# Kernel tuning notes

Hardware: AMD Instinct MI355X
Metric: run time of the kernel (lower is better)

## Reference

```python
import jax, jax.numpy as jnp
import numpy as np

N, E = 3200, 50000
RBF, HID = 16, 128
CUT = 5.0
NS, NV = 32, 16            # multiplicities of 0e and 1o blocks
D = NS + 3 * NV            # 80 = node/message irrep dim
WNUM = NS*NS + NV*NS + NS*NV + NV*NV  # 2304 tensor-product weights per edge
EPS = 1e-8
# path normalization (fully-connected TP, 2 paths per output irrep)
A1 = 1.0 / np.sqrt(2.0 * NS)
A2 = 1.0 / np.sqrt(2.0 * NV)
A3 = 1.0 / np.sqrt(2.0 * NS)
A4 = 1.0 / np.sqrt(2.0 * NV)
ISQ3 = 1.0 / np.sqrt(3.0)


def setup_inputs() -> dict:
    key = jax.random.key(0)
    ks = jax.random.split(key, 24)
    nrm = lambda k, s, sc=1.0: jax.random.normal(k, s, jnp.float32) * sc
    x = nrm(ks[0], (N, D))
    edge_src = jax.random.randint(ks[1], (E,), 0, N)
    edge_dst = jax.random.randint(ks[2], (E,), 0, N)
    dirs = nrm(ks[3], (E, 3))
    unit = dirs / jnp.linalg.norm(dirs, axis=1, keepdims=True)
    # component-normalized SH for l=0,1: [1, sqrt(3)*r_hat]
    edge_sh = jnp.concatenate([jnp.ones((E, 1), jnp.float32), np.sqrt(3.0) * unit], axis=1)
    edge_rbf = nrm(ks[4], (E, RBF))
    edge_len = jax.random.uniform(ks[5], (E,), jnp.float32, 0.1, 6.0)  # some beyond cutoff
    inp = dict(x=x, edge_src=edge_src, edge_dst=edge_dst, edge_sh=edge_sh,
               edge_rbf=edge_rbf, edge_len=edge_len)
    # IrrepNorm affine params
    inp['norm_w'] = jnp.ones((D,), jnp.float32)
    inp['norm_b'] = jnp.zeros((D,), jnp.float32)
    # radial weight MLP (RBF -> HID -> HID -> WNUM)
    inp['mw1'] = nrm(ks[6], (RBF, HID), 1.0/np.sqrt(RBF)); inp['mb1'] = jnp.zeros((HID,), jnp.float32)
    inp['mw2'] = nrm(ks[7], (HID, HID), 1.0/np.sqrt(HID)); inp['mb2'] = jnp.zeros((HID,), jnp.float32)
    inp['mw3'] = nrm(ks[8], (HID, WNUM), 1.0/np.sqrt(HID)); inp['mb3'] = jnp.zeros((WNUM,), jnp.float32)
    # edge gate MLP (RBF -> HID -> 1)
    inp['gw1'] = nrm(ks[9], (RBF, HID), 1.0/np.sqrt(RBF)); inp['gb1'] = jnp.zeros((HID,), jnp.float32)
    inp['gw2'] = nrm(ks[10], (HID, 1), 1.0/np.sqrt(HID)); inp['gb2'] = jnp.zeros((1,), jnp.float32)
    # equivariant linears (e3nn stores N(0,1) weights, normalizes by 1/sqrt(fan_in))
    inp['Ws'] = nrm(ks[11], (NS, NS + NV))   # msg_linear scalar part: 32 -> 32 scalars + 16 gates
    inp['Wv'] = nrm(ks[12], (NV, NV))        # msg_linear vector part
    inp['Us'] = nrm(ks[13], (NS, NS))        # update_linear
    inp['Uv'] = nrm(ks[14], (NV, NV))
    inp['Ss'] = nrm(ks[15], (NS, NS))        # self_linear
    inp['Sv'] = nrm(ks[16], (NV, NV))
    inp['res_scale'] = jnp.float32(0.1)
    return inp


def _irrep_norm(x, w, b):
    s = x[:, :NS]
    v = x[:, NS:].reshape(-1, NV, 3)
    mean = s.mean(axis=1, keepdims=True)
    var = ((s - mean) ** 2).mean(axis=1, keepdims=True)
    s = (s - mean) / jnp.sqrt(var + EPS)
    rms = jnp.sqrt((v ** 2).mean(axis=2, keepdims=True) + EPS)
    v = v / rms
    out = jnp.concatenate([s, v.reshape(-1, 3 * NV)], axis=-1)
    return out * w + b


def reference(x, edge_src, edge_dst, edge_sh, edge_rbf, edge_len,
              norm_w, norm_b, mw1, mb1, mw2, mb2, mw3, mb3,
              gw1, gb1, gw2, gb2, Ws, Wv, Us, Uv, Ss, Sv, res_scale):
    silu = jax.nn.silu
    x_norm = _irrep_norm(x, norm_w, norm_b)                  # [N, 80]
    # radial tensor-product weights per edge
    h = silu(edge_rbf @ mw1 + mb1)
    h = silu(h @ mw2 + mb2)
    tpw = h @ mw3 + mb3                                      # [E, 2304]
    o1 = NS*NS; o2 = o1 + NV*NS; o3 = o2 + NS*NV
    w1 = tpw[:, :o1].reshape(-1, NS, NS)
    w2 = tpw[:, o1:o2].reshape(-1, NV, NS)
    w3 = tpw[:, o2:o3].reshape(-1, NS, NV)
    w4 = tpw[:, o3:].reshape(-1, NV, NV)
    # gather source node features
    xs = x_norm[edge_src, :NS]                               # [E, 32]
    xv = x_norm[edge_src, NS:].reshape(-1, NV, 3)            # [E, 16, 3]
    sh0 = edge_sh[:, 0]                                      # [E]
    sh1 = edge_sh[:, 1:4]                                    # [E, 3]
    # fully-connected TP paths
    msg_s = A1 * jnp.einsum('ei,eio->eo', xs * sh0[:, None], w1)
    inner = jnp.einsum('eim,em->ei', xv, sh1) * ISQ3         # 1o x 1o -> 0e
    msg_s = msg_s + A2 * jnp.einsum('ei,eio->eo', inner, w2)
    msg_v = A3 * jnp.einsum('ei,eio->eo', xs, w3)[:, :, None] * sh1[:, None, :]
    msg_v = msg_v + A4 * jnp.einsum('eim,eio->eom', xv, w4) * sh0[:, None, None]
    m = jnp.concatenate([msg_s, msg_v.reshape(-1, 3 * NV)], axis=-1)  # [E, 80]
    # cutoff envelope and learned edge gate
    cutoff_w = 0.5 * (jnp.cos(jnp.pi * edge_len / CUT) + 1.0) * (edge_len <= CUT).astype(x.dtype)
    gate_w = jax.nn.sigmoid(silu(edge_rbf @ gw1 + gb1) @ gw2 + gb2)   # [E, 1]
    edge_w = cutoff_w[:, None] * gate_w                               # [E, 1]
    m = m * edge_w
    # scatter-add aggregate + normalization
    agg = jax.ops.segment_sum(m, edge_dst, num_segments=N)            # [N, 80]
    den = jax.ops.segment_sum(edge_w, edge_dst, num_segments=N)       # [N, 1]
    agg = agg / jnp.maximum(den, 1e-8)
    # msg_linear -> scalars + gates + gated vectors
    ag_s = agg[:, :NS]
    ag_v = agg[:, NS:].reshape(-1, NV, 3)
    sc = (ag_s @ Ws) / np.sqrt(NS)                                    # [N, 48]
    vc = jnp.einsum('nim,io->nom', ag_v, Wv) / np.sqrt(NV)            # [N, 16, 3]
    s_g = silu(sc[:, :NS])
    gates = jax.nn.sigmoid(sc[:, NS:])
    v_g = vc * gates[:, :, None]
    # update + self interaction
    upd_s = (s_g @ Us) / np.sqrt(NS)
    upd_v = jnp.einsum('nim,io->nom', v_g, Uv) / np.sqrt(NV)
    self_s = (x_norm[:, :NS] @ Ss) / np.sqrt(NS)
    self_v = jnp.einsum('nim,io->nom', x_norm[:, NS:].reshape(-1, NV, 3), Sv) / np.sqrt(NV)
    out = jnp.concatenate([self_s + upd_s, (self_v + upd_v).reshape(-1, 3 * NV)], axis=-1)
    return x + res_scale * out
```

## Files before the change

### kernel.cpp

```cpp
#include <hip/hip_runtime.h>
#include <hip/hip_bf16.h>
#include <math.h>

#define N_NODES 3200
#define E_EDGES 50000
#define RBFN 16
#define HID 128
#define NS 32
#define NV 16
#define DD 80
#define WNUM 2304
#define CUTF 5.0f
#define EPSF 1e-8f

#define A1C 0.125f
#define A2C 0.17677669529663687f
#define A3C 0.125f
#define A4C 0.17677669529663687f
#define A2ISQ 0.10206207261596575f

typedef __attribute__((ext_vector_type(4))) float f32x4;
typedef __attribute__((ext_vector_type(8))) short bf16x8;

__device__ __forceinline__ float sigm(float x) { return 1.0f / (1.0f + __expf(-x)); }
__device__ __forceinline__ float silu_f(float x) { return x * sigm(x); }

__device__ __forceinline__ short bf16r(float x) {
    union { float f; unsigned u; } v; v.f = x;
    unsigned r = (v.u + 0x7fffu + ((v.u >> 16) & 1u)) >> 16;
    return (short)r;
}
__device__ __forceinline__ float b2f(unsigned short s) {
    union { float f; unsigned u; } v; v.u = ((unsigned)s) << 16; return v.f;
}

__global__ void k_scan(const int* __restrict__ hist, int* __restrict__ start) {
    __shared__ int part[256];
    int t = threadIdx.x;
    int loc[13];
    int s = 0;
#pragma unroll
    for (int j = 0; j < 13; j++) {
        int idx = t * 13 + j;
        int v = (idx < N_NODES) ? hist[idx] : 0;
        loc[j] = s; s += v;
    }
    part[t] = s;
    __syncthreads();
    for (int off = 1; off < 256; off <<= 1) {
        int v = part[t];
        int add = (t >= off) ? part[t - off] : 0;
        __syncthreads();
        part[t] = v + add;
        __syncthreads();
    }
    int pre = (t == 0) ? 0 : part[t - 1];
#pragma unroll
    for (int j = 0; j < 13; j++) {
        int idx = t * 13 + j;
        if (idx < N_NODES) start[idx] = pre + loc[j];
    }
    if (t == 255) start[N_NODES] = part[255];
}

__global__ void k_scatter(const int* __restrict__ edst, const int* __restrict__ start,
                          int* __restrict__ cur, int* __restrict__ perm) {
    int e = blockIdx.x * 256 + threadIdx.x;
    if (e < E_EDGES) {
        int d = edst[e];
        int pos = start[d] + atomicAdd(&cur[d], 1);
        perm[pos] = e;
    }
}

__global__ void k_prep0(const float* __restrict__ mw2, __hip_bfloat16* __restrict__ mw2f) {
    __shared__ __hip_bfloat16 st[2048];
    int t = blockIdx.x, tid = threadIdx.x;
    for (int idx = tid; idx < 2048; idx += 256) {
        int k = idx >> 4, c = idx & 15;
        float v = mw2[k * HID + t * 16 + c];
        int kk = k >> 5, q4 = (k >> 3) & 3, j = k & 7;
        st[kk * 512 + (q4 * 16 + c) * 8 + j] = __float2bfloat16(v);
    }
    __syncthreads();
    ((bf16x8*)(mw2f + t * 2048))[tid] = ((const bf16x8*)st)[tid];
}

__global__ __launch_bounds__(256) void k_front(
    const float* __restrict__ rbf, const float* __restrict__ elen,
    const int* __restrict__ edst,
    const float* __restrict__ mw1, const float* __restrict__ mb1,
    const float* __restrict__ gw1, const float* __restrict__ gb1,
    const float* __restrict__ gw2, const float* __restrict__ gb2,
    const float* __restrict__ mb2, const __hip_bfloat16* __restrict__ mw2f,
    const float* __restrict__ mw3, const float* __restrict__ mb3,
    const float* __restrict__ x, const float* __restrict__ nw, const float* __restrict__ nb,
    float* __restrict__ ewg, __hip_bfloat16* __restrict__ h2b,
    __hip_bfloat16* __restrict__ mw3f, __hip_bfloat16* __restrict__ biasf,
    float* __restrict__ xn, int* __restrict__ hist) {
    __shared__ __align__(16) char smem[16640];
    int b = blockIdx.x, tid = threadIdx.x;
    if (b < 782) {
        __hip_bfloat16* h1l = (__hip_bfloat16*)smem;
        int wid = __builtin_amdgcn_readfirstlane(tid >> 6);
        int lane = tid & 63;
        int base = b * 64;
        int eb = base + wid * 16;
        {
            int c0 = lane, c1 = 64 + lane;
            float t0[16], t1[16], g0[16], g1[16];
            float b0 = mb1[c0], b1 = mb1[c1], gb0v = gb1[c0], gb1v = gb1[c1];
#pragma unroll
            for (int e = 0; e < 16; e++) { t0[e] = b0; t1[e] = b1; g0[e] = gb0v; g1[e] = gb1v; }
#pragma unroll
            for (int r = 0; r < RBFN; r++) {
                float w0 = mw1[r * HID + c0], w1 = mw1[r * HID + c1];
                float v0 = gw1[r * HID + c0], v1 = gw1[r * HID + c1];
#pragma unroll
                for (int e = 0; e < 16; e++) {
                    int ee = eb + e; if (ee >= E_EDGES) ee = E_EDGES - 1;
                    float rv = rbf[ee * RBFN + r];
                    t0[e] += rv * w0; t1[e] += rv * w1;
                    g0[e] += rv * v0; g1[e] += rv * v1;
                }
            }
            float q0 = gw2[c0], q1 = gw2[c1];
            float gb2v = gb2[0];
#pragma unroll
            for (int e = 0; e < 16; e++) {
                int le = wid * 16 + e;
                h1l[le * 128 + c0] = __float2bfloat16(silu_f(t0[e]));
                h1l[le * 128 + c1] = __float2bfloat16(silu_f(t1[e]));
                float p = silu_f(g0[e]) * q0 + silu_f(g1[e]) * q1;
                p += __shfl_xor(p, 1);  p += __shfl_xor(p, 2);  p += __shfl_xor(p, 4);
                p += __shfl_xor(p, 8);  p += __shfl_xor(p, 16); p += __shfl_xor(p, 32);
                if (lane == 0 && eb + e < E_EDGES) {
                    float len = elen[eb + e];
                    float cut = (len <= CUTF) ? 0.5f * (cosf(3.14159265358979f * len / CUTF) + 1.0f) : 0.f;
                    ewg[eb + e] = cut * sigm(p + gb2v);
                }
            }
        }
        __syncthreads();
        {
            int q4 = lane >> 4, l15 = lane & 15;
            int le = wid * 16 + l15;
            bf16x8 af[4];
#pragma unroll
            for (int kk = 0; kk < 4; kk++)
                af[kk] = *(const bf16x8*)(h1l + le * 128 + kk * 32 + q4 * 8);
            const f32x4 zf = {0.f, 0.f, 0.f, 0.f};
#pragma unroll
            for (int ct = 0; ct < 8; ct++) {
                f32x4 acc = zf;
#pragma unroll
                for (int kk = 0; kk < 4; kk++) {
                    bf16x8 bw = *(const bf16x8*)(mw2f + (ct * 4 + kk) * 512 + lane * 8);
                    acc = __builtin_amdgcn_mfma_f32_16x16x32_bf16(af[kk], bw, acc, 0, 0, 0);
                }
                float bias = mb2[ct * 16 + l15];
#pragma unroll
                for (int r = 0; r < 4; r++) {
                    int ge = base + wid * 16 + q4 * 4 + r;
                    if (ge < E_EDGES)
                        h2b[ge * HID + ct * 16 + l15] = __float2bfloat16(silu_f(acc[r] + bias));
                }
            }
        }
    } else if (b < 927) {
        int b2 = b - 782;
        __hip_bfloat16* st = (__hip_bfloat16*)smem;
        if (b2 < 144) {
            for (int idx = tid; idx < 2048; idx += 256) {
                int k = idx >> 4, c = idx & 15;
                float v = mw3[k * WNUM + b2 * 16 + c];
                int kk = k >> 5, q4 = (k >> 3) & 3, j = k & 7;
                st[kk * 512 + (q4 * 16 + c) * 8 + j] = __float2bfloat16(v);
            }
            __syncthreads();
            ((bf16x8*)(mw3f + b2 * 2048))[tid] = ((const bf16x8*)st)[tid];
        } else {
            for (int idx = tid; idx < 3072; idx += 256) {
                float val;
                if (idx < 1024) {
                    int oh = idx >> 9, l = (idx >> 3) & 63, j = idx & 7;
                    int o = oh * 16 + (l & 15), i = (l >> 4) * 8 + j;
                    val = mb3[i * 32 + o];
                } else if (idx < 2048) {
                    int t = idx - 1024;
                    int oh = t >> 9, l = (t >> 3) & 63, j = t & 7;
                    int o = oh * 16 + (l & 15), i = (l >> 4) * 8 + j;
                    val = (i < 16) ? mb3[1024 + i * 32 + o] : 0.f;
                } else if (idx < 2560) {
                    int t = idx - 2048;
                    int l = t >> 3, j = t & 7;
                    int o = l & 15, i = (l >> 4) * 8 + j;
                    val = mb3[1536 + i * 16 + o];
                } else {
                    int t = idx - 2560;
                    int l = t >> 3, j = t & 7;
                    int o = l & 15, i = (l >> 4) * 8 + j;
                    val = (i < 16) ? mb3[2048 + i * 16 + o] : 0.f;
                }
                biasf[idx] = __float2bfloat16(val);
            }
        }
    } else if (b < 1727) {
        float* row = (float*)smem;
        int sub = tid >> 6, t = tid & 63;
        int n = (b - 927) * 4 + sub;
        float* rw = row + sub * 80;
        const float* xr = x + n * DD;
        rw[t] = xr[t];
        if (t < 16) rw[64 + t] = xr[64 + t];
        __syncthreads();
        float mean = 0.f;
#pragma unroll
        for (int i = 0; i < NS; i++) mean += rw[i];
        mean *= (1.0f / NS);
        float var = 0.f;
#pragma unroll
        for (int i = 0; i < NS; i++) { float d = rw[i] - mean; var += d * d; }
        var *= (1.0f / NS);
        float inv = rsqrtf(var + EPSF);
        if (t < NS) xn[n * DD + t] = (rw[t] - mean) * inv * nw[t] + nb[t];
        if (t < 48) {
            int j = t / 3;
            float v0 = rw[NS + 3 * j], v1 = rw[NS + 3 * j + 1], v2 = rw[NS + 3 * j + 2];
            float rms = sqrtf((v0 * v0 + v1 * v1 + v2 * v2) * (1.0f / 3.0f) + EPSF);
            xn[n * DD + NS + t] = rw[NS + t] / rms * nw[NS + t] + nb[NS + t];
        }
    } else {
        int e = (b - 1727) * 256 + tid;
        if (e < E_EDGES) atomicAdd(&hist[edst[e]], 1);
    }
}

__global__ __launch_bounds__(256) void k_msg(
    const float* __restrict__ xn, const __hip_bfloat16* __restrict__ h2b,
    const float* __restrict__ ewg, const int* __restrict__ esrc,
    const int* __restrict__ edst, const int* __restrict__ perm,
    const float* __restrict__ esh,
    const __hip_bfloat16* __restrict__ mw3f, const __hip_bfloat16* __restrict__ biasf,
    const int* __restrict__ startp, float* __restrict__ agg, float* __restrict__ den) {
    __shared__ __align__(16) char pool[46080];
    unsigned short (*xng)[82]  = (unsigned short(*)[82])(pool);
    unsigned short (*innr)[16] = (unsigned short(*)[16])(pool + 20992);
    f32x4* lb0  = (f32x4*)(pool + 25088);
    f32x4* lb1  = (f32x4*)(pool + 25088 + 8192);
    float (*sh1l)[4] = (float(*)[4])(pool + 41472);
    float* sh0l = (float*)(pool + 43520);
    float* ewl  = (float*)(pool + 44032);
    int* dstl   = (int*)(pool + 44544);
    int* srcl   = (int*)(pool + 45056);
    int* gel    = (int*)(pool + 45568);
    float* msgl = (float*)(pool);

    const int tid = threadIdx.x;
    const int wid = __builtin_amdgcn_readfirstlane(tid >> 6);
    const int lane = tid & 63;
    const int q4 = lane >> 4;
    const int l15 = lane & 15;
    const int ib = q4 * 8;
    const int role = blockIdx.x & 1;
    const int e0 = (blockIdx.x >> 1) * 128;

    if (tid < 128) {
        int slot = e0 + tid;
        bool v = slot < E_EDGES;
        int ge = v ? perm[slot] : 0;
        gel[tid] = ge;
        srcl[tid] = esrc[ge];
        dstl[tid] = v ? edst[ge] : -1;
        ewl[tid] = v ? ewg[ge] : 0.f;
        sh0l[tid] = esh[ge * 4];
        sh1l[tid][0] = esh[ge * 4 + 1];
        sh1l[tid][1] = esh[ge * 4 + 2];
        sh1l[tid][2] = esh[ge * 4 + 3];
    }
    __syncthreads();
    for (int idx = tid; idx < 128 * 80; idx += 256) {
        int e = idx / 80, q = idx - e * 80;
        xng[e][q] = (unsigned short)bf16r(xn[srcl[e] * 80 + q]);
    }
    __syncthreads();
    if (role == 0) {
        for (int idx = tid; idx < 128 * 16; idx += 256) {
            int e = idx >> 4, i = idx & 15;
            float d = b2f(xng[e][32 + 3 * i]) * sh1l[e][0]
                    + b2f(xng[e][32 + 3 * i + 1]) * sh1l[e][1]
                    + b2f(xng[e][32 + 3 * i + 2]) * sh1l[e][2];
            innr[e][i] = (unsigned short)bf16r(A2ISQ * d);
        }
    }
    __syncthreads();

    int el[2] = { wid * 32 + l15, wid * 32 + 16 + l15 };
    bf16x8 hfr[2][4];
#pragma unroll
    for (int et = 0; et < 2; et++) {
        int ge = gel[el[et]];
        const __hip_bfloat16* hr = h2b + ge * HID;
#pragma unroll
        for (int kk = 0; kk < 4; kk++)
            hfr[et][kk] = *(const bf16x8*)(hr + kk * 32 + ib);
    }
    const f32x4 zf = {0.f, 0.f, 0.f, 0.f};
    float f1[2], f4e[2];
    f32x4 msgS[2][2], q3[2], qv[3][2];
    if (role == 0) {
#pragma unroll
        for (int et = 0; et < 2; et++) {
            f1[et] = A1C * sh0l[el[et]];
            bf16x8 p18, p28;
#pragma unroll
            for (int j = 0; j < 8; j++) {
                p18[j] = bf16r(b2f(xng[el[et]][ib + j]) * f1[et]);
                p28[j] = (ib + j < 16) ? (short)innr[el[et]][ib + j] : (short)0;
            }
            bf16x8 ba1a = *(const bf16x8*)(biasf + lane * 8);
            bf16x8 ba1b = *(const bf16x8*)(biasf + 512 + lane * 8);
            bf16x8 ba2a = *(const bf16x8*)(biasf + 1024 + lane * 8);
            bf16x8 ba2b = *(const bf16x8*)(biasf + 1536 + lane * 8);
            f32x4 a0 = __builtin_amdgcn_mfma_f32_16x16x32_bf16(ba1a, p18, zf, 0, 0, 0);
            msgS[0][et] = __builtin_amdgcn_mfma_f32_16x16x32_bf16(ba2a, p28, a0, 0, 0, 0);
            f32x4 a1 = __builtin_amdgcn_mfma_f32_16x16x32_bf16(ba1b, p18, zf, 0, 0, 0);
            msgS[1][et] = __builtin_amdgcn_mfma_f32_16x16x32_bf16(ba2b, p28, a1, 0, 0, 0);
        }
    } else {
#pragma unroll
        for (int et = 0; et < 2; et++) {
            f4e[et] = A4C * sh0l[el[et]];
            bf16x8 xs8;
#pragma unroll
            for (int j = 0; j < 8; j++) xs8[j] = (short)xng[el[et]][ib + j];
            bf16x8 ba3 = *(const bf16x8*)(biasf + 2048 + lane * 8);
            bf16x8 ba4 = *(const bf16x8*)(biasf + 2560 + lane * 8);
            q3[et] = __builtin_amdgcn_mfma_f32_16x16x32_bf16(ba3, xs8, zf, 0, 0, 0);
#pragma unroll
            for (int m = 0; m < 3; m++) {
                bf16x8 t8;
#pragma unroll
                for (int j = 0; j < 8; j++) {
                    int i = ib + j;
                    t8[j] = (i < 16) ? (short)xng[el[et]][32 + 3 * i + m] : (short)0;
                }
                qv[m][et] = __builtin_amdgcn_mfma_f32_16x16x32_bf16(ba4, t8, zf, 0, 0, 0);
            }
        }
    }

    const f32x4* gsrc = (const f32x4*)mw3f;

    auto compute_chunk = [&](int n, const __hip_bfloat16* bb) {
        f32x4 acc[2][2];
#pragma unroll
        for (int half = 0; half < 2; half++) {
            f32x4 a0 = zf, a1 = zf;
#pragma unroll
            for (int kk = 0; kk < 4; kk++) {
                bf16x8 af = *(const bf16x8*)(bb + ((half * 4 + kk) * 64 + lane) * 8);
                a0 = __builtin_amdgcn_mfma_f32_16x16x32_bf16(af, hfr[0][kk], a0, 0, 0, 0);
                a1 = __builtin_amdgcn_mfma_f32_16x16x32_bf16(af, hfr[1][kk], a1, 0, 0, 0);
            }
            acc[half][0] = a0; acc[half][1] = a1;
        }
        if (n < 32) {
            float p0 = f1[0] * b2f(xng[el[0]][n]);
            float p1 = f1[1] * b2f(xng[el[1]][n]);
#pragma unroll
            for (int half = 0; half < 2; half++)
#pragma unroll
                for (int r = 0; r < 4; r++) {
                    msgS[half][0][r] += p0 * acc[half][0][r];
                    msgS[half][1][r] += p1 * acc[half][1][r];
                }
        } else if (n < 48) {
            float p0 = b2f(innr[el[0]][n - 32]);
            float p1 = b2f(innr[el[1]][n - 32]);
#pragma unroll
            for (int half = 0; half < 2; half++)
#pragma unroll
                for (int r = 0; r < 4; r++) {
                    msgS[half][0][r] += p0 * acc[half][0][r];
                    msgS[half][1][r] += p1 * acc[half][1][r];
                }
        } else if (n < 64) {
#pragma unroll
            for (int half = 0; half < 2; half++) {
                int i = 2 * (n - 48) + half;
                float p0 = b2f(xng[el[0]][i]);
                float p1 = b2f(xng[el[1]][i]);
#pragma unroll
                for (int r = 0; r < 4; r++) {
                    q3[0][r] += p0 * acc[half][0][r];
                    q3[1][r] += p1 * acc[half][1][r];
                }
            }
        } else {
#pragma unroll
            for (int half = 0; half < 2; half++) {
                int i = 2 * (n - 64) + half;
#pragma unroll
                for (int m = 0; m < 3; m++) {
                    float p0 = b2f(xng[el[0]][32 + 3 * i + m]);
                    float p1 = b2f(xng[el[1]][32 + 3 * i + m]);
#pragma unroll
                    for (int r = 0; r < 4; r++) {
                        qv[m][0][r] += p0 * acc[half][0][r];
                        qv[m][1][r] += p1 * acc[half][1][r];
                    }
                }
            }
        }
    };

    const int n0 = role ? 48 : 0;
    const int n1 = role ? 72 : 48;
    f32x4 rg0, rg1;
    rg0 = gsrc[n0 * 512 + tid];
    rg1 = gsrc[n0 * 512 + 256 + tid];
    {
        f32x4* wb = (n0 & 1) ? lb1 : lb0;
        wb[tid] = rg0; wb[tid + 256] = rg1;
        if (n0 + 1 < n1) {
            rg0 = gsrc[(n0 + 1) * 512 + tid];
            rg1 = gsrc[(n0 + 1) * 512 + 256 + tid];
        }
    }
    for (int n = n0; n < n1; n++) {
        __syncthreads();
        const __hip_bfloat16* bb = (const __hip_bfloat16*)((n & 1) ? lb1 : lb0);
        compute_chunk(n, bb);
        if (n + 1 < n1) {
            f32x4* wb = ((n + 1) & 1) ? lb1 : lb0;
            wb[tid] = rg0; wb[tid + 256] = rg1;
            if (n + 2 < n1) {
                rg0 = gsrc[(n + 2) * 512 + tid];
                rg1 = gsrc[(n + 2) * 512 + 256 + tid];
            }
        }
    }

    __syncthreads();
    if (role == 0) {
#pragma unroll
        for (int et = 0; et < 2; et++) {
            int le = el[et];
            float ew = ewl[le];
#pragma unroll
            for (int oh = 0; oh < 2; oh++)
#pragma unroll
                for (int r = 0; r < 4; r++)
                    msgl[le * 48 + oh * 16 + q4 * 4 + r] = msgS[oh][et][r] * ew;
        }
    } else {
#pragma unroll
        for (int et = 0; et < 2; et++) {
            int le = el[et];
            float ew = ewl[le];
            float s0 = sh1l[le][0], s1 = sh1l[le][1], s2 = sh1l[le][2];
            float b4 = f4e[et];
#pragma unroll
            for (int r = 0; r < 4; r++) {
                int o = q4 * 4 + r;
                float qq = A3C * q3[et][r];
                msgl[le * 48 + o * 3 + 0] = (qq * s0 + b4 * qv[0][et][r]) * ew;
                msgl[le * 48 + o * 3 + 1] = (qq * s1 + b4 * qv[1][et][r]) * ew;
                msgl[le * 48 + o * 3 + 2] = (qq * s2 + b4 * qv[2][et][r]) * ew;
            }
        }
    }
    __syncthreads();

    int nch = role ? 48 : 33;
    if (tid < nch) {
        int c = tid;
        int cnt = E_EDGES - e0; if (cnt > 128) cnt = 128;
        int cur = dstl[0];
        float acc = 0.f;
        for (int r = 0; r < cnt; r++) {
            int nd = dstl[r];
            if (nd != cur) {
                if (cur >= 0) {
                    bool interior = (startp[cur] >= e0) && (startp[cur + 1] <= e0 + 128);
                    float* p = (role == 0) ? ((c == 32) ? (den + cur) : (agg + cur * 80 + c))
                                           : (agg + cur * 80 + 32 + c);
                    if (interior) *p = acc; else atomicAdd(p, acc);
                }
                acc = 0.f; cur = nd;
            }
            acc += (role == 0 && c == 32) ? ewl[r] : msgl[r * 48 + c];
        }
        if (cur >= 0) {
            bool interior = (startp[cur] >= e0) && (startp[cur + 1] <= e0 + 128);
            float* p = (role == 0) ? ((c == 32) ? (den + cur) : (agg + cur * 80 + c))
                                   : (agg + cur * 80 + 32 + c);
            if (interior) *p = acc; else atomicAdd(p, acc);
        }
    }
}

__global__ void k_update(
    const float* __restrict__ x, const float* __restrict__ xn,
    const float* __restrict__ agg, const float* __restrict__ den,
    const float* __restrict__ Ws, const float* __restrict__ Wv,
    const float* __restrict__ Us, const float* __restrict__ Uv,
    const float* __restrict__ Ss, const float* __restrict__ Sv,
    const float* __restrict__ rsp, float* __restrict__ out) {
    int n = blockIdx.x, t = threadIdx.x;
    __shared__ float ag[DD];
    __shared__ float xnl[DD];
    __shared__ float sg[NS];
    __shared__ float gt[NV];
    __shared__ float vg[48];
    float idv = 1.0f / fmaxf(den[n], 1e-8f);
    ag[t] = agg[n * DD + t] * idv;
    if (t < 16) ag[64 + t] = agg[n * DD + 64 + t] * idv;
    xnl[t] = xn[n * DD + t];
    if (t < 16) xnl[64 + t] = xn[n * DD + 64 + t];
    __syncthreads();
    const float iqs = 0.17677669529663687f;
    const float iqv = 0.25f;
    if (t < 48) {
        float acc = 0.f;
#pragma unroll
        for (int i = 0; i < NS; i++) acc += ag[i] * Ws[i * 48 + t];
        acc *= iqs;
        if (t < NS) sg[t] = silu_f(acc);
        else gt[t - NS] = sigm(acc);
    }
    __syncthreads();
    if (t < 48) {
        int o = t / 3, m = t - 3 * o;
        float acc = 0.f;
#pragma unroll
        for (int i = 0; i < NV; i++) acc += ag[NS + 3 * i + m] * Wv[i * NV + o];
        vg[t] = acc * iqv * gt[o];
    }
    __syncthreads();
    float rs = rsp[0];
    if (t < NS) {
        float us = 0.f, ss = 0.f;
#pragma unroll
        for (int i = 0; i < NS; i++) { us += sg[i] * Us[i * NS + t]; ss += xnl[i] * Ss[i * NS + t]; }
        out[n * DD + t] = x[n * DD + t] + rs * ((ss + us) * iqs);
    }
    if (t < 48) {
        int o = t / 3, m = t - 3 * o;
        float uv = 0.f, sv = 0.f;
#pragma unroll
        for (int i = 0; i < NV; i++) { uv += vg[3 * i + m] * Uv[i * NV + o]; sv += xnl[NS + 3 * i + m] * Sv[i * NV + o]; }
        out[n * DD + NS + t] = x[n * DD + NS + t] + rs * ((sv + uv) * iqv);
    }
}

extern "C" void kernel_launch(void* const* d_in, const int* in_sizes, int n_in,
                              void* d_out, int out_size, void* d_ws, size_t ws_size,
                              hipStream_t stream) {
    (void)in_sizes; (void)n_in; (void)out_size; (void)ws_size;
    const float* x    = (const float*)d_in[0];
    const int*   esrc = (const int*)d_in[1];
    const int*   edst = (const int*)d_in[2];
    const float* esh  = (const float*)d_in[3];
    const float* erbf = (const float*)d_in[4];
    const float* elen = (const float*)d_in[5];
    const float* nw   = (const float*)d_in[6];
    const float* nb   = (const float*)d_in[7];
    const float* mw1  = (const float*)d_in[8];
    const float* mb1  = (const float*)d_in[9];
    const float* mw2  = (const float*)d_in[10];
    const float* mb2  = (const float*)d_in[11];
    const float* mw3  = (const float*)d_in[12];
    const float* mb3  = (const float*)d_in[13];
    const float* gw1  = (const float*)d_in[14];
    const float* gb1  = (const float*)d_in[15];
    const float* gw2  = (const float*)d_in[16];
    const float* gb2  = (const float*)d_in[17];
    const float* Ws   = (const float*)d_in[18];
    const float* Wv   = (const float*)d_in[19];
    const float* Us   = (const float*)d_in[20];
    const float* Uv   = (const float*)d_in[21];
    const float* Ss   = (const float*)d_in[22];
    const float* Sv   = (const float*)d_in[23];
    const float* rsp  = (const float*)d_in[24];
    float* out = (float*)d_out;
    float* ws  = (float*)d_ws;

    float* agg    = ws;
    float* den    = ws + 256000;
    int*   hist   = (int*)(ws + 259200);
    int*   cur    = (int*)(ws + 262400);
    int*   startp = (int*)(ws + 265600);
    int*   perm   = (int*)(ws + 268801);
    float* xn     = ws + 318804;
    float* ewg    = ws + 574804;
    __hip_bfloat16* h2b   = (__hip_bfloat16*)(ws + 624804);
    __hip_bfloat16* mw3f  = (__hip_bfloat16*)(ws + 3824804);
    __hip_bfloat16* biasf = (__hip_bfloat16*)(ws + 3972260);
    __hip_bfloat16* mw2f  = (__hip_bfloat16*)(ws + 3973796);

    hipMemsetAsync(ws, 0, 265600 * sizeof(float), stream);
    k_prep0<<<8, 256, 0, stream>>>(mw2, mw2f);
    k_front<<<1923, 256, 0, stream>>>(erbf, elen, edst, mw1, mb1, gw1, gb1, gw2, gb2,
                                      mb2, mw2f, mw3, mb3, x, nw, nb,
                                      ewg, h2b, mw3f, biasf, xn, hist);
    k_scan<<<1, 256, 0, stream>>>(hist, startp);
    k_scatter<<<196, 256, 0, stream>>>(edst, startp, cur, perm);
    k_msg<<<782, 256, 0, stream>>>(xn, h2b, ewg, esrc, edst, perm, esh,
                                   mw3f, biasf, startp, agg, den);
    k_update<<<N_NODES, 64, 0, stream>>>(x, xn, agg, den, Ws, Wv, Us, Uv, Ss, Sv, rsp, out);
}
```

Baseline: 280.8 us.

## Rebalance weight chunks evenly between the two block roles with atomic scalar scatter

Changes the split of radial-weight chunks so each block role handles 36 of the 72 chunks instead of 48 and 24. Because the vector-role blocks now also accumulate part of the scalar outputs, both roles now add scalar channels into the aggregate with atomics. The innr precompute therefore runs for both roles, and the vector role gets an extra staging and scatter pass. The next chunk's LDS store is also moved before the compute of the current chunk in the double-buffered loop. The aim is to even out work between the two block kinds, at the cost of more atomics and an extra reduction pass.

```diff
diff --git a/kernel.cpp b/kernel.cpp
--- a/kernel.cpp
+++ b/kernel.cpp
@@ -284,14 +284,12 @@
         xng[e][q] = (unsigned short)bf16r(xn[srcl[e] * 80 + q]);
     }
     __syncthreads();
-    if (role == 0) {
-        for (int idx = tid; idx < 128 * 16; idx += 256) {
-            int e = idx >> 4, i = idx & 15;
-            float d = b2f(xng[e][32 + 3 * i]) * sh1l[e][0]
-                    + b2f(xng[e][32 + 3 * i + 1]) * sh1l[e][1]
-                    + b2f(xng[e][32 + 3 * i + 2]) * sh1l[e][2];
-            innr[e][i] = (unsigned short)bf16r(A2ISQ * d);
-        }
+    for (int idx = tid; idx < 128 * 16; idx += 256) {
+        int e = idx >> 4, i = idx & 15;
+        float d = b2f(xng[e][32 + 3 * i]) * sh1l[e][0]
+                + b2f(xng[e][32 + 3 * i + 1]) * sh1l[e][1]
+                + b2f(xng[e][32 + 3 * i + 2]) * sh1l[e][2];
+        innr[e][i] = (unsigned short)bf16r(A2ISQ * d);
     }
     __syncthreads();
 
@@ -308,10 +306,16 @@
     const f32x4 zf = {0.f, 0.f, 0.f, 0.f};
     float f1[2], f4e[2];
     f32x4 msgS[2][2], q3[2], qv[3][2];
+#pragma unroll
+    for (int et = 0; et < 2; et++) {
+        f1[et] = A1C * sh0l[el[et]];
+        f4e[et] = A4C * sh0l[el[et]];
+        msgS[0][et] = zf; msgS[1][et] = zf;
+        q3[et] = zf; qv[0][et] = zf; qv[1][et] = zf; qv[2][et] = zf;
+    }
     if (role == 0) {
 #pragma unroll
         for (int et = 0; et < 2; et++) {
-            f1[et] = A1C * sh0l[el[et]];
             bf16x8 p18, p28;
 #pragma unroll
             for (int j = 0; j < 8; j++) {
@@ -330,7 +334,6 @@
     } else {
 #pragma unroll
         for (int et = 0; et < 2; et++) {
-            f4e[et] = A4C * sh0l[el[et]];
             bf16x8 xs8;
 #pragma unroll
             for (int j = 0; j < 8; j++) xs8[j] = (short)xng[el[et]][ib + j];
@@ -415,23 +418,18 @@
         }
     };
 
-    const int n0 = role ? 48 : 0;
-    const int n1 = role ? 72 : 48;
-    f32x4 rg0, rg1;
-    rg0 = gsrc[n0 * 512 + tid];
-    rg1 = gsrc[n0 * 512 + 256 + tid];
+    const int n0 = role ? 36 : 0;
+    const int n1 = role ? 72 : 36;
+    f32x4 rg0 = gsrc[n0 * 512 + tid];
+    f32x4 rg1 = gsrc[n0 * 512 + 256 + tid];
     {
         f32x4* wb = (n0 & 1) ? lb1 : lb0;
         wb[tid] = rg0; wb[tid + 256] = rg1;
-        if (n0 + 1 < n1) {
-            rg0 = gsrc[(n0 + 1) * 512 + tid];
-            rg1 = gsrc[(n0 + 1) * 512 + 256 + tid];
-        }
+        rg0 = gsrc[(n0 + 1) * 512 + tid];
+        rg1 = gsrc[(n0 + 1) * 512 + 256 + tid];
     }
     for (int n = n0; n < n1; n++) {
         __syncthreads();
-        const __hip_bfloat16* bb = (const __hip_bfloat16*)((n & 1) ? lb1 : lb0);
-        compute_chunk(n, bb);
         if (n + 1 < n1) {
             f32x4* wb = ((n + 1) & 1) ? lb1 : lb0;
             wb[tid] = rg0; wb[tid + 256] = rg1;
@@ -440,9 +438,11 @@
                 rg1 = gsrc[(n + 2) * 512 + 256 + tid];
             }
         }
-    }
-
-    __syncthreads();
+        compute_chunk(n, (const __hip_bfloat16*)((n & 1) ? lb1 : lb0));
+    }
+
+    __syncthreads();
+    int cnt = E_EDGES - e0; if (cnt > 128) cnt = 128;
     if (role == 0) {
 #pragma unroll
         for (int et = 0; et < 2; et++) {
@@ -454,7 +454,62 @@
                 for (int r = 0; r < 4; r++)
                     msgl[le * 48 + oh * 16 + q4 * 4 + r] = msgS[oh][et][r] * ew;
         }
+        __syncthreads();
+        if (tid < 33) {
+            int c = tid;
+            int cur = dstl[0];
+            float acc = 0.f;
+            for (int r = 0; r < cnt; r++) {
+                int nd = dstl[r];
+                if (nd != cur) {
+                    if (cur >= 0) {
+                        if (c == 32) {
+                            bool interior = (startp[cur] >= e0) && (startp[cur + 1] <= e0 + 128);
+                            if (interior) den[cur] = acc; else atomicAdd(den + cur, acc);
+                        } else {
+                            atomicAdd(agg + cur * 80 + c, acc);
+                        }
+                    }
+                    acc = 0.f; cur = nd;
+                }
+                acc += (c == 32) ? ewl[r] : msgl[r * 48 + c];
+            }
+            if (cur >= 0) {
+                if (c == 32) {
+                    bool interior = (startp[cur] >= e0) && (startp[cur + 1] <= e0 + 128);
+                    if (interior) den[cur] = acc; else atomicAdd(den + cur, acc);
+                } else {
+                    atomicAdd(agg + cur * 80 + c, acc);
+                }
+            }
+        }
     } else {
+#pragma unroll
+        for (int et = 0; et < 2; et++) {
+            int le = el[et];
+            float ew = ewl[le];
+#pragma unroll
+            for (int oh = 0; oh < 2; oh++)
+#pragma unroll
+                for (int r = 0; r < 4; r++)
+                    msgl[le * 48 + oh * 16 + q4 * 4 + r] = msgS[oh][et][r] * ew;
+        }
+        __syncthreads();
+        if (tid < 32) {
+            int c = tid;
+            int cur = dstl[0];
+            float acc = 0.f;
+            for (int r = 0; r < cnt; r++) {
+                int nd = dstl[r];
+                if (nd != cur) {
+                    if (cur >= 0) atomicAdd(agg + cur * 80 + c, acc);
+                    acc = 0.f; cur = nd;
+                }
+                acc += msgl[r * 48 + c];
+            }
+            if (cur >= 0) atomicAdd(agg + cur * 80 + c, acc);
+        }
+        __syncthreads();
 #pragma unroll
         for (int et = 0; et < 2; et++) {
             int le = el[et];
@@ -470,33 +525,28 @@
                 msgl[le * 48 + o * 3 + 2] = (qq * s2 + b4 * qv[2][et][r]) * ew;
             }
         }
-    }
-    __syncthreads();
-
-    int nch = role ? 48 : 33;
-    if (tid < nch) {
-        int c = tid;
-        int cnt = E_EDGES - e0; if (cnt > 128) cnt = 128;
-        int cur = dstl[0];
-        float acc = 0.f;
-        for (int r = 0; r < cnt; r++) {
-            int nd = dstl[r];
-            if (nd != cur) {
-                if (cur >= 0) {
-                    bool interior = (startp[cur] >= e0) && (startp[cur + 1] <= e0 + 128);
-                    float* p = (role == 0) ? ((c == 32) ? (den + cur) : (agg + cur * 80 + c))
-                                           : (agg + cur * 80 + 32 + c);
-                    if (interior) *p = acc; else atomicAdd(p, acc);
-                }
-                acc = 0.f; cur = nd;
-            }
-            acc += (role == 0 && c == 32) ? ewl[r] : msgl[r * 48 + c];
-        }
-        if (cur >= 0) {
-            bool interior = (startp[cur] >= e0) && (startp[cur + 1] <= e0 + 128);
-            float* p = (role == 0) ? ((c == 32) ? (den + cur) : (agg + cur * 80 + c))
-                                   : (agg + cur * 80 + 32 + c);
-            if (interior) *p = acc; else atomicAdd(p, acc);
+        __syncthreads();
+        if (tid < 48) {
+            int c = tid;
+            int cur = dstl[0];
+            float acc = 0.f;
+            for (int r = 0; r < cnt; r++) {
+                int nd = dstl[r];
+                if (nd != cur) {
+                    if (cur >= 0) {
+                        bool interior = (startp[cur] >= e0) && (startp[cur + 1] <= e0 + 128);
+                        float* p = agg + cur * 80 + 32 + c;
+                        if (interior) *p = acc; else atomicAdd(p, acc);
+                    }
+                    acc = 0.f; cur = nd;
+                }
+                acc += msgl[r * 48 + c];
+            }
+            if (cur >= 0) {
+                bool interior = (startp[cur] >= e0) && (startp[cur + 1] <= e0 + 128);
+                float* p = agg + cur * 80 + 32 + c;
+                if (interior) *p = acc; else atomicAdd(p, acc);
+            }
         }
     }
 }
```

After: 282.2 us. Within noise of the previous version (+0.5%).
